# Kernel tuning notes

Hardware: AMD Instinct MI355X
Metric: run time of the kernel (lower is better)

Reference implementation:

```python
import jax, jax.numpy as jnp
import numpy as np


def fwht(x):
    """Fast Walsh-Hadamard transform over last axis (power-of-2 length), normalized by 1/sqrt(n).
    Matches matmul_hadU with K=1 (pure Hadamard rotation)."""
    orig_shape = x.shape
    n = orig_shape[-1]
    x = x.reshape(-1, n)
    h = 1
    while h < n:
        x = x.reshape(-1, n // (2 * h), 2, h)
        a = x[:, :, 0, :]
        b = x[:, :, 1, :]
        x = jnp.stack([a + b, a - b], axis=2)
        h *= 2
    x = x.reshape(orig_shape)
    return x * (1.0 / np.sqrt(n)).astype(np.float32)


def setup_inputs() -> dict:
    key = jax.random.key(0)
    k1, k2, k3, k4, k5 = jax.random.split(key, 5)
    B, S, n, m = 2, 2048, 4096, 4096
    CODEBOOK = 65536  # 2^16 E8P codes, each decoding an 8-dim lattice point
    inp = jax.random.normal(k1, (B, S, n), dtype=jnp.float32)
    # SU/SV are random sign-like diagonal rescales in QuIP; use unit-variance floats here
    SU = jax.random.normal(k2, (n,), dtype=jnp.float32)
    SV = jax.random.normal(k3, (m,), dtype=jnp.float32)
    grid = jax.random.normal(k4, (CODEBOOK, 8), dtype=jnp.float32) * 0.1
    Qidxs = jax.random.randint(k5, (m, n // 8), 0, CODEBOOK, dtype=jnp.int32)
    return {"input": inp, "SU": SU, "SV": SV, "grid": grid, "Qidxs": Qidxs}


def reference(input, SU, SV, grid, Qidxs):
    n = SU.shape[0]
    m = SV.shape[0]
    x = input.reshape(-1, n) * SU          # diagonal rescale by SU
    x = fwht(x)                             # left Hadamard rotation
    # Dequantize packed E8P codebook: each 16-bit code -> 8 weights
    W = grid[Qidxs].reshape(m, n)           # [m, n]
    x = x @ W.T                             # dense GEMM against dequantized weight
    x = fwht(x)                             # right Hadamard rotation
    x = x * SV                              # diagonal rescale by SV
    return x.reshape(input.shape[:-1] + (m,))
```

## Files before the change

kernel.cpp:

```cpp
#include <hip/hip_runtime.h>
#include <stdint.h>

typedef __bf16 bf16x8 __attribute__((ext_vector_type(8)));
typedef float f32x4 __attribute__((ext_vector_type(4)));

__device__ __forceinline__ unsigned int f2bf(float f) {
  unsigned int u = __float_as_uint(f);
  return (u + 0x7fffu + ((u >> 16) & 1u)) >> 16;
}
__device__ __forceinline__ unsigned int pack2(float a, float b) {
  return f2bf(a) | (f2bf(b) << 16);
}

__device__ __forceinline__ void fwht16(float v[16]) {
#pragma unroll
  for (int s = 0; s < 4; ++s) {
    const int h = 1 << s;
#pragma unroll
    for (int i = 0; i < 16; ++i) {
      if (!(i & h)) {
        float a = v[i], b = v[i ^ h];
        v[i] = a + b;
        v[i ^ h] = a - b;
      }
    }
  }
}

#define LP(i) ((i) + ((i) >> 5))

__global__ void __launch_bounds__(256) k_fwht_in(const float* __restrict__ X,
                                                 const float* __restrict__ SU,
                                                 unsigned short* __restrict__ Xh) {
  __shared__ float lds[4224];
  const int t = threadIdx.x;
  const size_t row = blockIdx.x;
  const float4* xr = (const float4*)(X + row * 4096);
  const float4* su = (const float4*)SU;
  float v[16];
#pragma unroll
  for (int q = 0; q < 4; ++q) {
    float4 a = xr[4 * t + q], s = su[4 * t + q];
    v[4 * q + 0] = a.x * s.x;
    v[4 * q + 1] = a.y * s.y;
    v[4 * q + 2] = a.z * s.z;
    v[4 * q + 3] = a.w * s.w;
  }
  fwht16(v);
#pragma unroll
  for (int q = 0; q < 4; ++q) {
    int i0 = 16 * t + 4 * q;
    *(float4*)&lds[LP(i0)] = make_float4(v[4 * q], v[4 * q + 1], v[4 * q + 2], v[4 * q + 3]);
  }
  __syncthreads();
  const int b = ((t >> 4) << 8) | (t & 15);
#pragma unroll
  for (int j = 0; j < 16; ++j) { int i = b + 16 * j; v[j] = lds[LP(i)]; }
  fwht16(v);
#pragma unroll
  for (int j = 0; j < 16; ++j) { int i = b + 16 * j; lds[LP(i)] = v[j]; }
  __syncthreads();
#pragma unroll
  for (int j = 0; j < 16; ++j) { int i = t + 256 * j; v[j] = lds[LP(i)]; }
  fwht16(v);
  unsigned short* orow = Xh + row * 4096;
#pragma unroll
  for (int j = 0; j < 16; ++j)
    orow[t + 256 * j] = (unsigned short)f2bf(v[j] * 0.015625f);
}

__global__ void __launch_bounds__(256) k_decompress(const int* __restrict__ Qidxs,
                                                    const float* __restrict__ G,
                                                    unsigned short* __restrict__ Wh) {
  int e = blockIdx.x * 256 + threadIdx.x;
  int idx = Qidxs[e];
  const float4* g = (const float4*)(G + (size_t)idx * 8);
  float4 a = g[0], b = g[1];
  uint4 o;
  o.x = pack2(a.x, a.y);
  o.y = pack2(a.z, a.w);
  o.z = pack2(b.x, b.y);
  o.w = pack2(b.z, b.w);
  ((uint4*)Wh)[e] = o;
}

__device__ __forceinline__ void gl2lds16(const unsigned short* g, unsigned short* l) {
  __builtin_amdgcn_global_load_lds(
      (const __attribute__((address_space(1))) void*)g,
      (__attribute__((address_space(3))) void*)l, 16, 0, 0);
}

#define BARX() __builtin_amdgcn_s_barrier()
#define SCHEDB() __builtin_amdgcn_sched_barrier(0)
#define WAITL0() asm volatile("s_waitcnt lgkmcnt(0)" ::: "memory")
#define WAITV4() asm volatile("s_waitcnt vmcnt(4)" ::: "memory")

#define APHASE(q, STMT, TAIL)                                                   \
  {                                                                             \
    bf16x8 af[2][2];                                                            \
    _Pragma("unroll") for (int mm = 0; mm < 2; ++mm)                            \
        _Pragma("unroll") for (int kh = 0; kh < 2; ++kh)                        \
            af[mm][kh] = *(const bf16x8*)&sAp[((wr << 7) + (((q)*2 + mm) << 4) + frow) * 64 + \
                                              ((((kh << 2) + jb) ^ sw) << 3)];  \
    STMT;                                                                       \
    BARX();                                                                     \
    WAITL0();                                                                   \
    SCHEDB();                                                                   \
    __builtin_amdgcn_s_setprio(1);                                              \
    _Pragma("unroll") for (int mm = 0; mm < 2; ++mm)                            \
        _Pragma("unroll") for (int n = 0; n < 4; ++n)                           \
            _Pragma("unroll") for (int kh = 0; kh < 2; ++kh)                    \
                acc[(q)*2 + mm][n] = __builtin_amdgcn_mfma_f32_16x16x32_bf16(   \
                    af[mm][kh], bq[n][kh], acc[(q)*2 + mm][n], 0, 0, 0);        \
    __builtin_amdgcn_s_setprio(0);                                              \
    TAIL;                                                                       \
    BARX();                                                                     \
    SCHEDB();                                                                   \
  }

__global__ void __launch_bounds__(512, 2)
k_gemm_bt(const unsigned short* __restrict__ A,
          const unsigned short* __restrict__ B,
          float* __restrict__ C) {
  const int K = 4096, N = 4096;
  __shared__ unsigned short sA[2][256 * 64];
  __shared__ unsigned short sB[2][256 * 64];
  const int tid = threadIdx.x;
  const int lane = tid & 63;
  const int wave = tid >> 6;
  const int wr = wave >> 2;
  const int wc = wave & 3;
  const int frow = lane & 15;
  const int jb = lane >> 4;
  const int sw = frow & 7;
  const int bn = blockIdx.x, bm = blockIdx.y;
  const size_t rowA0 = (size_t)bm * 256;
  const size_t rowB0 = (size_t)bn * 256;

  f32x4 acc[8][4] = {};

  auto stage = [&](const unsigned short* __restrict__ G, size_t row0,
                   unsigned short* dst, int h, int ktile) {
    const int kt = (ktile < 64 ? ktile : 0) << 6;
#pragma unroll
    for (int l = 0; l < 2; ++l) {
      const int c = (l << 9) + tid;
      const int r = c >> 3;
      const int jg = (c & 7) ^ (r & 7);
      gl2lds16(G + (row0 + (size_t)((h << 7) + r)) * K + kt + (jg << 3),
               dst + (h << 13) + (c << 3));
    }
  };

  auto group = [&](int p, int gA, int gB) {
    const unsigned short* sAp = sA[p];
    const unsigned short* sBp = sB[p];
    unsigned short* sAn = sA[p ^ 1];
    unsigned short* sBn = sB[p];
    bf16x8 bq[4][2];
#pragma unroll
    for (int n = 0; n < 4; ++n)
#pragma unroll
      for (int kh = 0; kh < 2; ++kh)
        bq[n][kh] = *(const bf16x8*)&sBp[((wc << 6) + (n << 4) + frow) * 64 +
                                         ((((kh << 2) + jb) ^ sw) << 3)];
    APHASE(0, (stage(A, rowA0, sAn, 0, gA)), ((void)0));
    APHASE(1, (stage(A, rowA0, sAn, 1, gA)), ((void)0));
    APHASE(2, (stage(B, rowB0, sBn, 0, gB)), ((void)0));
    APHASE(3, (stage(B, rowB0, sBn, 1, gB)), WAITV4());
  };

  stage(B, rowB0, sB[0], 0, 0);
  stage(B, rowB0, sB[0], 1, 0);
  stage(A, rowA0, sA[0], 0, 0);
  stage(A, rowA0, sA[0], 1, 0);
  stage(B, rowB0, sB[1], 0, 1);
  stage(B, rowB0, sB[1], 1, 1);
  WAITV4();
  BARX();
  SCHEDB();

#pragma unroll 1
  for (int i = 0; i < 32; ++i) {
    group(0, 2 * i + 1, 2 * i + 2);
    group(1, 2 * i + 2, 2 * i + 3);
  }

  const int rbase = bm * 256 + (wr << 7) + (jb << 2);
  const int cbase = bn * 256 + (wc << 6) + frow;
#pragma unroll
  for (int m = 0; m < 8; ++m)
#pragma unroll
    for (int n = 0; n < 4; ++n) {
      float* cp = C + (size_t)(rbase + (m << 4)) * N + cbase + (n << 4);
#pragma unroll
      for (int r = 0; r < 4; ++r) cp[(size_t)r * N] = acc[m][n][r];
    }
}

__global__ void __launch_bounds__(256) k_fwht_out(float* __restrict__ Y,
                                                  const float* __restrict__ SV) {
  __shared__ float lds[4224];
  const int t = threadIdx.x;
  const size_t row = blockIdx.x;
  float* yrow = Y + row * 4096;
  const float4* yr = (const float4*)yrow;
  float v[16];
#pragma unroll
  for (int q = 0; q < 4; ++q) {
    float4 a = yr[4 * t + q];
    v[4 * q + 0] = a.x;
    v[4 * q + 1] = a.y;
    v[4 * q + 2] = a.z;
    v[4 * q + 3] = a.w;
  }
  fwht16(v);
#pragma unroll
  for (int q = 0; q < 4; ++q) {
    int i0 = 16 * t + 4 * q;
    *(float4*)&lds[LP(i0)] = make_float4(v[4 * q], v[4 * q + 1], v[4 * q + 2], v[4 * q + 3]);
  }
  __syncthreads();
  const int b = ((t >> 4) << 8) | (t & 15);
#pragma unroll
  for (int j = 0; j < 16; ++j) { int i = b + 16 * j; v[j] = lds[LP(i)]; }
  fwht16(v);
#pragma unroll
  for (int j = 0; j < 16; ++j) { int i = b + 16 * j; lds[LP(i)] = v[j]; }
  __syncthreads();
#pragma unroll
  for (int j = 0; j < 16; ++j) { int i = t + 256 * j; v[j] = lds[LP(i)]; }
  fwht16(v);
#pragma unroll
  for (int j = 0; j < 16; ++j) {
    int i = t + 256 * j;
    yrow[i] = v[j] * SV[i] * 0.015625f;
  }
}

extern "C" void kernel_launch(void* const* d_in, const int* in_sizes, int n_in,
                              void* d_out, int out_size, void* d_ws, size_t ws_size,
                              hipStream_t stream) {
  const float* X     = (const float*)d_in[0];
  const float* SU    = (const float*)d_in[1];
  const float* SV    = (const float*)d_in[2];
  const float* G     = (const float*)d_in[3];
  const int*   Qidxs = (const int*)d_in[4];
  float* out = (float*)d_out;

  unsigned short* Xh = (unsigned short*)d_ws;
  unsigned short* Wh = Xh + (size_t)4096 * 4096;

  k_fwht_in<<<4096, 256, 0, stream>>>(X, SU, Xh);
  k_decompress<<<(4096 * 512) / 256, 256, 0, stream>>>(Qidxs, G, Wh);
  k_gemm_bt<<<dim3(16, 16), 512, 0, stream>>>(Xh, Wh, out);
  k_fwht_out<<<4096, 256, 0, stream>>>(out, SV);
}
```

Before: 280.4 us.

## Software-pipeline LDS A-fragment reads with MFMA using double register buffers

Restructures the per-k-tile group so A fragments are read from LDS into two alternating register buffers, with the next fragment loaded while MFMAs on the current one run. The explicit lgkmcnt(0) wait before each MFMA block is removed, and barriers and vmcnt waits are reshuffled (vmcnt 4 then vmcnt 2) to order the global-to-LDS staging. The aim is to hide LDS read latency behind matrix math. The cost is more live registers and a more delicate barrier and wait ordering around buffer reuse.

```diff
diff --git a/kernel.cpp b/kernel.cpp
--- a/kernel.cpp
+++ b/kernel.cpp
@@ -92,31 +92,23 @@
 
 #define BARX() __builtin_amdgcn_s_barrier()
 #define SCHEDB() __builtin_amdgcn_sched_barrier(0)
-#define WAITL0() asm volatile("s_waitcnt lgkmcnt(0)" ::: "memory")
 #define WAITV4() asm volatile("s_waitcnt vmcnt(4)" ::: "memory")
-
-#define APHASE(q, STMT, TAIL)                                                   \
-  {                                                                             \
-    bf16x8 af[2][2];                                                            \
-    _Pragma("unroll") for (int mm = 0; mm < 2; ++mm)                            \
-        _Pragma("unroll") for (int kh = 0; kh < 2; ++kh)                        \
-            af[mm][kh] = *(const bf16x8*)&sAp[((wr << 7) + (((q)*2 + mm) << 4) + frow) * 64 + \
-                                              ((((kh << 2) + jb) ^ sw) << 3)];  \
-    STMT;                                                                       \
-    BARX();                                                                     \
-    WAITL0();                                                                   \
-    SCHEDB();                                                                   \
-    __builtin_amdgcn_s_setprio(1);                                              \
-    _Pragma("unroll") for (int mm = 0; mm < 2; ++mm)                            \
-        _Pragma("unroll") for (int n = 0; n < 4; ++n)                           \
-            _Pragma("unroll") for (int kh = 0; kh < 2; ++kh)                    \
-                acc[(q)*2 + mm][n] = __builtin_amdgcn_mfma_f32_16x16x32_bf16(   \
-                    af[mm][kh], bq[n][kh], acc[(q)*2 + mm][n], 0, 0, 0);        \
-    __builtin_amdgcn_s_setprio(0);                                              \
-    TAIL;                                                                       \
-    BARX();                                                                     \
-    SCHEDB();                                                                   \
-  }
+#define WAITV2() asm volatile("s_waitcnt vmcnt(2)" ::: "memory")
+
+#define RD_A(dst, mm)                                                          \
+  _Pragma("unroll") for (int kh = 0; kh < 2; ++kh)                             \
+      dst[kh] = *(const bf16x8*)&sAp[(((wr) << 7) + ((mm) << 4) + frow) * 64 + \
+                                     ((((kh << 2) + jb) ^ sw) << 3)];
+#define RD_B()                                                                 \
+  _Pragma("unroll") for (int n = 0; n < 4; ++n)                                \
+      _Pragma("unroll") for (int kh = 0; kh < 2; ++kh)                         \
+          bq[n][kh] = *(const bf16x8*)&sBp[(((wc) << 6) + (n << 4) + frow) * 64 + \
+                                           ((((kh << 2) + jb) ^ sw) << 3)];
+#define MF(mm, buf)                                                            \
+  _Pragma("unroll") for (int n = 0; n < 4; ++n)                                \
+      _Pragma("unroll") for (int kh = 0; kh < 2; ++kh)                         \
+          acc[(mm)][n] = __builtin_amdgcn_mfma_f32_16x16x32_bf16(              \
+              buf[kh], bq[n][kh], acc[(mm)][n], 0, 0, 0);
 
 __global__ void __launch_bounds__(512, 2)
 k_gemm_bt(const unsigned short* __restrict__ A,
@@ -155,19 +147,49 @@
   auto group = [&](int p, int gA, int gB) {
     const unsigned short* sAp = sA[p];
     const unsigned short* sBp = sB[p];
-    unsigned short* sAn = sA[p ^ 1];
-    unsigned short* sBn = sB[p];
+    unsigned short* sAn = (unsigned short*)sA[p ^ 1];
+    unsigned short* sBn = (unsigned short*)sB[p];
     bf16x8 bq[4][2];
-#pragma unroll
-    for (int n = 0; n < 4; ++n)
-#pragma unroll
-      for (int kh = 0; kh < 2; ++kh)
-        bq[n][kh] = *(const bf16x8*)&sBp[((wc << 6) + (n << 4) + frow) * 64 +
-                                         ((((kh << 2) + jb) ^ sw) << 3)];
-    APHASE(0, (stage(A, rowA0, sAn, 0, gA)), ((void)0));
-    APHASE(1, (stage(A, rowA0, sAn, 1, gA)), ((void)0));
-    APHASE(2, (stage(B, rowB0, sBn, 0, gB)), ((void)0));
-    APHASE(3, (stage(B, rowB0, sBn, 1, gB)), WAITV4());
+    bf16x8 aX[2], aY[2];
+    RD_B();
+    RD_A(aX, 0);
+    RD_A(aY, 1);
+    stage(A, rowA0, sAn, 0, gA);
+    BARX(); SCHEDB();
+    __builtin_amdgcn_s_setprio(1);
+    MF(0, aX);
+    RD_A(aX, 2);
+    MF(1, aY);
+    __builtin_amdgcn_s_setprio(0);
+    BARX(); SCHEDB();
+    RD_A(aY, 3);
+    stage(A, rowA0, sAn, 1, gA);
+    BARX(); SCHEDB();
+    __builtin_amdgcn_s_setprio(1);
+    MF(2, aX);
+    RD_A(aX, 4);
+    MF(3, aY);
+    __builtin_amdgcn_s_setprio(0);
+    WAITV4(); SCHEDB();
+    BARX(); SCHEDB();
+    RD_A(aY, 5);
+    stage(B, rowB0, sBn, 0, gB);
+    BARX(); SCHEDB();
+    __builtin_amdgcn_s_setprio(1);
+    MF(4, aX);
+    RD_A(aX, 6);
+    MF(5, aY);
+    __builtin_amdgcn_s_setprio(0);
+    WAITV2(); SCHEDB();
+    BARX(); SCHEDB();
+    RD_A(aY, 7);
+    stage(B, rowB0, sBn, 1, gB);
+    BARX(); SCHEDB();
+    __builtin_amdgcn_s_setprio(1);
+    MF(6, aX);
+    MF(7, aY);
+    __builtin_amdgcn_s_setprio(0);
+    BARX(); SCHEDB();
   };
 
   stage(B, rowB0, sB[0], 0, 0);
```

Measured after the change: 272.0 us. 1.03x faster.
